# Kernel tuning notes

Measured on AMD Instinct MI355X. Metric: run time of the kernel, lower is better.

The kernel has to match this reference:

```python
import jax, jax.numpy as jnp
import numpy as np

N = 50000
E = 800000
IN_F = 256
ATT_D = 256
H = 8
D_K = ATT_D // H  # 32
NORM_IDX = 0  # opt['attention_norm_idx']


def setup_inputs() -> dict:
    key = jax.random.key(0)
    ks = jax.random.split(key, 10)
    x = jax.random.normal(ks[0], (N, IN_F), dtype=jnp.float32)
    edge = jax.random.randint(ks[1], (2, E), 0, N, dtype=jnp.int64)
    edge_weights = jax.random.uniform(ks[2], (E,), dtype=jnp.float32)
    s = 0.02
    Wq = jax.random.normal(ks[3], (ATT_D, IN_F), dtype=jnp.float32) * s
    bq = jax.random.normal(ks[4], (ATT_D,), dtype=jnp.float32) * s
    Wk = jax.random.normal(ks[5], (ATT_D, IN_F), dtype=jnp.float32) * s
    bk = jax.random.normal(ks[6], (ATT_D,), dtype=jnp.float32) * s
    Wv = jax.random.normal(ks[7], (ATT_D, IN_F), dtype=jnp.float32) * s
    bv = jax.random.normal(ks[8], (ATT_D,), dtype=jnp.float32) * s
    return {"x": x, "edge": edge, "edge_weights": edge_weights,
            "Wq": Wq, "bq": bq, "Wk": Wk, "bk": bk, "Wv": Wv, "bv": bv}


def _segment_softmax(logits, seg, num_segments):
    # scatter-softmax grouped by seg (torch_geometric.utils.softmax semantics)
    m = jax.ops.segment_max(logits, seg, num_segments=num_segments)  # [N, H]
    ex = jnp.exp(logits - m[seg])
    s = jax.ops.segment_sum(ex, seg, num_segments=num_segments)
    return ex / (s[seg] + 1e-16)


def reference(x, edge, edge_weights, Wq, bq, Wk, bk, Wv, bv):
    # Linear projections, then [N, H, D_K] -> transpose to [N, D_K, H]
    q = (x @ Wq.T + bq).reshape(N, H, D_K).transpose(0, 2, 1)
    k = (x @ Wk.T + bk).reshape(N, H, D_K).transpose(0, 2, 1)
    v = (x @ Wv.T + bv).reshape(N, H, D_K).transpose(0, 2, 1)
    src = q[edge[0]]      # [E, D_K, H]
    dst_k = k[edge[1]]    # [E, D_K, H]
    prods = jnp.sum(src * dst_k, axis=1) / np.sqrt(D_K)  # [E, H]
    prods = prods * edge_weights[:, None]
    attention = _segment_softmax(prods, edge[NORM_IDX], N)  # [E, H]
    return attention, v
```

## Files before the change

### kernel.cpp

```cpp
#include <hip/hip_runtime.h>

#define NN 50000
#define EE 800000
#define FF 256
#define HH 8
#define DK 32

typedef short bf16x8 __attribute__((ext_vector_type(8)));
typedef float f32x4  __attribute__((ext_vector_type(4)));

__device__ __forceinline__ float b2f(short s) {
    return __uint_as_float(((unsigned)(unsigned short)s) << 16);
}
__device__ __forceinline__ short f2b(float f) {
    unsigned u = __float_as_uint(f);
    return (short)((u + 0x7fff + ((u >> 16) & 1)) >> 16);
}

__device__ __forceinline__ void gld16(void* lds, const void* g) {
    __builtin_amdgcn_global_load_lds(
        (const __attribute__((address_space(1))) unsigned int*)g,
        (__attribute__((address_space(3))) unsigned int*)lds,
        16, 0, 0);
}

__global__ __launch_bounds__(256) void sniff_all(
    const void* x, const void* ew, const void* wq, const void* bq,
    const void* wk, const void* bk, const void* wv, const void* bv,
    const void* edge, int* __restrict__ flags)
{
    __shared__ int tot;
    if (threadIdx.x == 0) tot = 0;
    __syncthreads();
    int b = blockIdx.x;
    if (b < 8) {
        const void* ptrs[8] = {x, ew, wq, bq, wk, bk, wv, bv};
        const int   ns[8]   = {NN * FF, EE, FF * FF, FF, FF * FF, FF, FF * FF, FF};
        const unsigned short* p = (const unsigned short*)ptrs[b];
        int half = ns[b] >> 1;
        int S = half < 4096 ? half : 4096;
        int cnt = 0;
        for (int i = threadIdx.x; i < S; i += 256) {
            unsigned v = p[2 * i];
            cnt += (((v >> 7) & 0xFF) >= 0xC0) ? 1 : 0;
        }
        atomicAdd(&tot, cnt);
        __syncthreads();
        if (threadIdx.x == 0) flags[b] = (tot * 32 > S) ? 1 : 0;
    } else {
        const unsigned* e32 = (const unsigned*)edge;
        int cnt = 0;
        for (int i = threadIdx.x; i < 4096; i += 256)
            cnt += (e32[2 * i + 1] != 0u) ? 1 : 0;
        atomicAdd(&tot, cnt);
        __syncthreads();
        if (threadIdx.x == 0) flags[8] = (tot < 100) ? 1 : 0;
    }
}

__global__ __launch_bounds__(256) void convert_wb(
    const void* wq, const void* wk, const void* wv,
    const void* bq, const void* bk, const void* bv,
    short* __restrict__ wb, float* __restrict__ bb,
    const int* __restrict__ flags)
{
    int b = blockIdx.x;
    if (b < 96) {
        int mat = b >> 5;
        const void* src = mat == 0 ? wq : mat == 1 ? wk : wv;
        int isf = flags[2 + mat * 2];
        int base = (b & 31) * 2048 + threadIdx.x * 8;
        bf16x8 v;
        if (isf) {
            const f32x4* pp = (const f32x4*)((const float*)src + base);
            f32x4 a = pp[0], c = pp[1];
            #pragma unroll
            for (int j = 0; j < 4; ++j) { v[j] = f2b(a[j]); v[4 + j] = f2b(c[j]); }
        } else {
            v = *(const bf16x8*)((const short*)src + base);
        }
        int row = base >> 8, k = base & 255;
        int s = k >> 5, quad = (k >> 3) & 3;
        int pc = (row << 2) + (quad ^ ((row >> 1) & 3));
        *(bf16x8*)(wb + mat * (FF * FF) + s * 8192 + pc * 8) = v;
    } else {
        #pragma unroll
        for (int mat = 0; mat < 3; ++mat) {
            const void* src = mat == 0 ? bq : mat == 1 ? bk : bv;
            int isf = flags[3 + mat * 2];
            int i = threadIdx.x;
            bb[mat * FF + i] = isf ? ((const float*)src)[i]
                                   : b2f(((const short*)src)[i]);
        }
    }
}

__global__ __launch_bounds__(256) void qkv_gemm(
    const void* __restrict__ x, const short* __restrict__ wb,
    const float* __restrict__ bb, short* __restrict__ qo,
    short* __restrict__ ko, float* __restrict__ vo,
    const int* __restrict__ flags, int mlo, int mhi)
{
    __shared__ __align__(16) short wlds[2][8192];
    const int isf32x = flags[0];
    const int tid = threadIdx.x, wave = tid >> 6, lane = tid & 63;
    const int l16 = lane & 15, quad = lane >> 4;
    const int rows0 = blockIdx.x * 64 + wave * 16;
    const int rowa = rows0 + l16;
    const int rowc = rowa < NN ? rowa : NN - 1;
    const int koff = quad * 8;
    const size_t xrow = (size_t)rowc * FF;

    const int rdo = l16 * 32 + ((quad ^ ((l16 >> 1) & 3)) << 3);

    bf16x8 afrag[8];
    if (isf32x) {
        f32x4 t0[8], t1[8];
        #pragma unroll
        for (int s = 0; s < 8; ++s) {
            const f32x4* p = (const f32x4*)((const float*)x + xrow + s * 32 + koff);
            t0[s] = p[0]; t1[s] = p[1];
        }
        #pragma unroll
        for (int s = 0; s < 8; ++s)
            #pragma unroll
            for (int j = 0; j < 4; ++j) {
                afrag[s][j]     = f2b(t0[s][j]);
                afrag[s][4 + j] = f2b(t1[s][j]);
            }
    } else {
        #pragma unroll
        for (int s = 0; s < 8; ++s)
            afrag[s] = *(const bf16x8*)((const short*)x + xrow + s * 32 + koff);
    }

    #define STAGE(buf, W_, s) do {                                              \
        const short* gs_ = (W_) + (s) * 8192;                                   \
        _Pragma("unroll")                                                       \
        for (int i_ = 0; i_ < 4; ++i_)                                          \
            gld16(&wlds[buf][(i_ * 256 + (tid & ~63)) * 8],                     \
                  gs_ + (size_t)(i_ * 256 + tid) * 8);                          \
    } while (0)

    for (int mat = mlo; mat <= mhi; ++mat) {
        const short* W = wb + mat * (FF * FF);
        if (mat != mlo) __syncthreads();
        STAGE(0, W, 0);
        __syncthreads();

        f32x4 acc[16] = {};
        #pragma unroll
        for (int s = 0; s < 8; ++s) {
            const int cur = s & 1;
            if (s < 7) STAGE(cur ^ 1, W, s + 1);
            const short* ws0 = &wlds[cur][rdo];
            #pragma unroll
            for (int c = 0; c < 16; ++c) {
                bf16x8 bf = *(const bf16x8*)(ws0 + c * 512);
                acc[c] = __builtin_amdgcn_mfma_f32_16x16x32_bf16(afrag[s], bf, acc[c], 0, 0, 0);
            }
            __syncthreads();
        }

        const float* bias = bb + mat * FF;
        short* slice = (short*)wlds + wave * 4096;

        if (mat == 2) {
            float* lsf = (float*)slice;
            #pragma unroll
            for (int h = 0; h < 2; ++h) {
                #pragma unroll
                for (int ci = 0; ci < 8; ++ci) {
                    int c = ci * 2 + h;
                    int col = c * 16 + l16;
                    float bv = bias[col];
                    int pcl = l16 * 8 + ci;
                    #pragma unroll
                    for (int rr = 0; rr < 4; ++rr)
                        lsf[(quad * 4 + rr) * 128 + pcl] = acc[c][rr] + bv;
                }
                #pragma unroll
                for (int it = 0; it < 8; ++it) {
                    int idx = it * 64 + lane;
                    int r = idx >> 5, cc = idx & 31;
                    int row = rows0 + r;
                    if (row < NN)
                        *(f32x4*)(vo + (size_t)row * FF + h * 128 + cc * 4) =
                            ((const f32x4*)lsf)[idx];
                }
            }
        } else {
            #pragma unroll
            for (int c = 0; c < 16; ++c) {
                int col = c * 16 + l16;
                float bv = bias[col];
                #pragma unroll
                for (int rr = 0; rr < 4; ++rr)
                    slice[(quad * 4 + rr) * 256 + col] = f2b(acc[c][rr] + bv);
            }
            short* out = (mat == 0) ? qo : ko;
            #pragma unroll
            for (int it = 0; it < 8; ++it) {
                int idx = it * 64 + lane;
                int r = idx >> 5, cc = idx & 31;
                int row = rows0 + r;
                if (row < NN)
                    *(bf16x8*)(out + (size_t)row * FF + cc * 8) =
                        *(const bf16x8*)(slice + r * 256 + cc * 8);
            }
        }
    }
    #undef STAGE
}

__device__ __forceinline__ float edge_exp_f(
    const int* __restrict__ edge, const void* __restrict__ ew,
    const short* __restrict__ q, const short* __restrict__ k,
    int t, int isf32, int is64, int* s_out)
{
    int e = t >> 3, h = t & 7;
    int s = is64 ? edge[2 * (size_t)e] : edge[e];
    int d = is64 ? edge[2 * ((size_t)EE + e)] : edge[EE + e];
    *s_out = s;
    const short* qp = q + (size_t)s * FF + h * DK;
    const short* kp = k + (size_t)d * FF + h * DK;
    float dot = 0.f;
    #pragma unroll
    for (int i = 0; i < 4; ++i) {
        bf16x8 qa = *(const bf16x8*)(qp + i * 8);
        bf16x8 ka = *(const bf16x8*)(kp + i * 8);
        #pragma unroll
        for (int j = 0; j < 8; ++j) dot += b2f(qa[j]) * b2f(ka[j]);
    }
    float w = isf32 ? ((const float*)ew)[e] : b2f(((const short*)ew)[e]);
    return __expf(dot * 0.17677669529663687f * w);
}

__global__ __launch_bounds__(256) void edge_pass_a(
    const int* __restrict__ edge, const void* __restrict__ ew,
    const short* __restrict__ q, const short* __restrict__ k,
    float* __restrict__ sums, float* __restrict__ expbuf,
    const int* __restrict__ flags, int use_exp)
{
    int t = blockIdx.x * 256 + threadIdx.x;
    int s;
    float exv = edge_exp_f(edge, ew, q, k, t, flags[1], flags[8], &s);
    if (use_exp) expbuf[t] = exv;
    atomicAdd(&sums[s * HH + (threadIdx.x & 7)], exv);
}

__global__ __launch_bounds__(256) void rsum_inv(float* __restrict__ sums)
{
    int i = blockIdx.x * 256 + threadIdx.x;
    if (i < NN * HH) sums[i] = 1.0f / (sums[i] + 1e-16f);
}

__global__ __launch_bounds__(256) void edge_pass_b(
    const int* __restrict__ edge, const void* __restrict__ ew,
    const short* __restrict__ q, const short* __restrict__ k,
    const float* __restrict__ sums, const float* __restrict__ expbuf,
    float* __restrict__ att, const int* __restrict__ flags, int use_exp)
{
    int t = blockIdx.x * 256 + threadIdx.x;
    float exv; int s;
    if (use_exp) {
        int e = t >> 3;
        s = flags[8] ? edge[2 * (size_t)e] : edge[e];
        exv = expbuf[t];
    } else {
        exv = edge_exp_f(edge, ew, q, k, t, flags[1], flags[8], &s);
    }
    att[t] = exv * sums[s * HH + (t & 7)];
}

extern "C" void kernel_launch(void* const* d_in, const int* in_sizes, int n_in,
                              void* d_out, int out_size, void* d_ws, size_t ws_size,
                              hipStream_t stream) {
    const void* x    = d_in[0];
    const int*  edge = (const int*)d_in[1];
    const void* ew   = d_in[2];
    const void* Wq   = d_in[3];
    const void* bq   = d_in[4];
    const void* Wk   = d_in[5];
    const void* bk   = d_in[6];
    const void* Wv   = d_in[7];
    const void* bv   = d_in[8];

    float* att_out = (float*)d_out;
    float* v_out   = att_out + (size_t)EE * HH;

    char*  ws    = (char*)d_ws;
    int*   flags = (int*)ws;
    float* sums  = (float*)(ws + 256);
    const size_t SUMS_B = (size_t)NN * HH * 4;
    const size_t Q_B    = (size_t)NN * FF * 2;
    const size_t EXP_B  = (size_t)EE * HH * 4;
    short* q_  = (short*)(ws + 256 + SUMS_B);
    short* wb  = (short*)(ws + 256 + SUMS_B + Q_B);
    float* bb  = (float*)(ws + 256 + SUMS_B + Q_B + 3 * FF * FF * 2);
    float* expb = (float*)(ws + 256 + SUMS_B + Q_B + 3 * FF * FF * 2 + 3 * FF * 4);
    const size_t BASE_B = 256 + SUMS_B + Q_B + 3 * FF * FF * 2 + 3 * FF * 4;
    const int use_exp = (ws_size >= BASE_B + EXP_B) ? 1 : 0;
    const int fused   = (ws_size >= BASE_B + EXP_B + Q_B) ? 1 : 0;

    sniff_all<<<9, 256, 0, stream>>>(x, ew, Wq, bq, Wk, bk, Wv, bv, edge, flags);
    convert_wb<<<97, 256, 0, stream>>>(Wq, Wk, Wv, bq, bk, bv, wb, bb, flags);
    hipMemsetAsync(sums, 0, SUMS_B, stream);

    const int nEH = EE * HH;
    dim3 g((NN + 63) / 64);

    if (fused) {
        short* k_ = (short*)(ws + BASE_B + EXP_B);
        qkv_gemm<<<g, 256, 0, stream>>>(x, wb, bb, q_, k_, v_out, flags, 0, 2);
        edge_pass_a<<<nEH / 256, 256, 0, stream>>>(edge, ew, q_, k_, sums, expb, flags, 1);
        rsum_inv<<<(NN * HH + 255) / 256, 256, 0, stream>>>(sums);
        edge_pass_b<<<nEH / 256, 256, 0, stream>>>(edge, ew, q_, k_, sums, expb, att_out, flags, 1);
    } else {
        short* k_ = (short*)v_out;
        qkv_gemm<<<g, 256, 0, stream>>>(x, wb, bb, q_, k_, nullptr, flags, 0, 1);
        edge_pass_a<<<nEH / 256, 256, 0, stream>>>(edge, ew, q_, k_, sums, expb, flags, use_exp);
        rsum_inv<<<(NN * HH + 255) / 256, 256, 0, stream>>>(sums);
        edge_pass_b<<<nEH / 256, 256, 0, stream>>>(edge, ew, q_, k_, sums, expb, att_out, flags, use_exp);
        qkv_gemm<<<g, 256, 0, stream>>>(x, wb, bb, nullptr, nullptr, v_out, flags, 2, 2);
    }
}
```

Measured before the change: 336.7 us.

## Split QKV GEMM across blocks per matrix with XCD-aware block swizzle

The QKV projection kernel now assigns each workgroup a single 64-row tile of one weight matrix instead of looping over all three, launching 3x as many 128-thread blocks. Each wave handles 32 rows (two 16-row MFMA fragments sharing each B-fragment LDS read), and block IDs are remapped so neighbouring tiles land on the same XCD for L2 reuse of x. The aim is more parallelism and better weight-fragment reuse per LDS load. The cost is that x rows are reloaded and converted once per matrix rather than once per tile, and there is higher register pressure from doubled accumulators.

```diff
diff --git a/kernel.cpp b/kernel.cpp
--- a/kernel.cpp
+++ b/kernel.cpp
@@ -22,6 +22,12 @@
         (const __attribute__((address_space(1))) unsigned int*)g,
         (__attribute__((address_space(3))) unsigned int*)lds,
         16, 0, 0);
+}
+
+__device__ __forceinline__ int xcd_swz(int bid, int nwg) {
+    int q = nwg >> 3, r = nwg & 7, x = bid & 7, i = bid >> 3;
+    int base = x < r ? x * (q + 1) : r * (q + 1) + (x - r) * q;
+    return base + i;
 }
 
 __global__ __launch_bounds__(256) void sniff_all(
@@ -95,80 +101,88 @@
     }
 }
 
-__global__ __launch_bounds__(256) void qkv_gemm(
+__global__ __launch_bounds__(128, 2) void qkv_gemm(
     const void* __restrict__ x, const short* __restrict__ wb,
     const float* __restrict__ bb, short* __restrict__ qo,
     short* __restrict__ ko, float* __restrict__ vo,
-    const int* __restrict__ flags, int mlo, int mhi)
+    const int* __restrict__ flags, int matbase, int nmats)
 {
     __shared__ __align__(16) short wlds[2][8192];
     const int isf32x = flags[0];
     const int tid = threadIdx.x, wave = tid >> 6, lane = tid & 63;
     const int l16 = lane & 15, quad = lane >> 4;
-    const int rows0 = blockIdx.x * 64 + wave * 16;
-    const int rowa = rows0 + l16;
-    const int rowc = rowa < NN ? rowa : NN - 1;
+
+    const int nwg = 782 * nmats;
+    const int w = xcd_swz(blockIdx.x, nwg);
+    const int xb = w / nmats;
+    const int mat = matbase + (w - xb * nmats);
+
+    const short* W = wb + mat * (FF * FF);
+    const int rows0 = xb * 64 + wave * 32;
+
+    const int rdo = l16 * 32 + ((quad ^ ((l16 >> 1) & 3)) << 3);
     const int koff = quad * 8;
-    const size_t xrow = (size_t)rowc * FF;
-
-    const int rdo = l16 * 32 + ((quad ^ ((l16 >> 1) & 3)) << 3);
-
-    bf16x8 afrag[8];
-    if (isf32x) {
-        f32x4 t0[8], t1[8];
-        #pragma unroll
-        for (int s = 0; s < 8; ++s) {
-            const f32x4* p = (const f32x4*)((const float*)x + xrow + s * 32 + koff);
-            t0[s] = p[0]; t1[s] = p[1];
-        }
-        #pragma unroll
-        for (int s = 0; s < 8; ++s)
-            #pragma unroll
-            for (int j = 0; j < 4; ++j) {
-                afrag[s][j]     = f2b(t0[s][j]);
-                afrag[s][4 + j] = f2b(t1[s][j]);
+
+    bf16x8 afrag[2][8];
+    #pragma unroll
+    for (int rg = 0; rg < 2; ++rg) {
+        const int rowa = rows0 + rg * 16 + l16;
+        const int rowc = rowa < NN ? rowa : NN - 1;
+        const size_t xrow = (size_t)rowc * FF;
+        if (isf32x) {
+            #pragma unroll
+            for (int s = 0; s < 8; ++s) {
+                const f32x4* p = (const f32x4*)((const float*)x + xrow + s * 32 + koff);
+                f32x4 u = p[0], v2 = p[1];
+                #pragma unroll
+                for (int j = 0; j < 4; ++j) {
+                    afrag[rg][s][j]     = f2b(u[j]);
+                    afrag[rg][s][4 + j] = f2b(v2[j]);
+                }
             }
-    } else {
-        #pragma unroll
-        for (int s = 0; s < 8; ++s)
-            afrag[s] = *(const bf16x8*)((const short*)x + xrow + s * 32 + koff);
-    }
-
-    #define STAGE(buf, W_, s) do {                                              \
-        const short* gs_ = (W_) + (s) * 8192;                                   \
+        } else {
+            #pragma unroll
+            for (int s = 0; s < 8; ++s)
+                afrag[rg][s] = *(const bf16x8*)((const short*)x + xrow + s * 32 + koff);
+        }
+    }
+
+    #define STAGE(buf, s) do {                                                  \
+        const short* gs_ = W + (s) * 8192;                                      \
         _Pragma("unroll")                                                       \
-        for (int i_ = 0; i_ < 4; ++i_)                                          \
-            gld16(&wlds[buf][(i_ * 256 + (tid & ~63)) * 8],                     \
-                  gs_ + (size_t)(i_ * 256 + tid) * 8);                          \
+        for (int i_ = 0; i_ < 8; ++i_)                                          \
+            gld16(&wlds[buf][(i_ * 128 + (tid & ~63)) * 8],                     \
+                  gs_ + (size_t)(i_ * 128 + tid) * 8);                          \
     } while (0)
 
-    for (int mat = mlo; mat <= mhi; ++mat) {
-        const short* W = wb + mat * (FF * FF);
-        if (mat != mlo) __syncthreads();
-        STAGE(0, W, 0);
+    STAGE(0, 0);
+    __syncthreads();
+
+    f32x4 acc[2][16] = {};
+    #pragma unroll
+    for (int s = 0; s < 8; ++s) {
+        const int cur = s & 1;
+        if (s < 7) STAGE(cur ^ 1, s + 1);
+        const short* ws0 = &wlds[cur][rdo];
+        #pragma unroll
+        for (int c = 0; c < 16; ++c) {
+            bf16x8 bf = *(const bf16x8*)(ws0 + c * 512);
+            acc[0][c] = __builtin_amdgcn_mfma_f32_16x16x32_bf16(afrag[0][s], bf, acc[0][c], 0, 0, 0);
+            acc[1][c] = __builtin_amdgcn_mfma_f32_16x16x32_bf16(afrag[1][s], bf, acc[1][c], 0, 0, 0);
+        }
         __syncthreads();
-
-        f32x4 acc[16] = {};
-        #pragma unroll
-        for (int s = 0; s < 8; ++s) {
-            const int cur = s & 1;
-            if (s < 7) STAGE(cur ^ 1, W, s + 1);
-            const short* ws0 = &wlds[cur][rdo];
-            #pragma unroll
-            for (int c = 0; c < 16; ++c) {
-                bf16x8 bf = *(const bf16x8*)(ws0 + c * 512);
-                acc[c] = __builtin_amdgcn_mfma_f32_16x16x32_bf16(afrag[s], bf, acc[c], 0, 0, 0);
-            }
-            __syncthreads();
-        }
-
-        const float* bias = bb + mat * FF;
-        short* slice = (short*)wlds + wave * 4096;
-
-        if (mat == 2) {
-            float* lsf = (float*)slice;
-            #pragma unroll
-            for (int h = 0; h < 2; ++h) {
+    }
+    #undef STAGE
+
+    const float* bias = bb + mat * FF;
+    short* slice = (short*)wlds + wave * 8192;
+
+    if (mat == 2) {
+        float* lsf = (float*)slice;
+        #pragma unroll
+        for (int h = 0; h < 2; ++h) {
+            #pragma unroll
+            for (int rg = 0; rg < 2; ++rg)
                 #pragma unroll
                 for (int ci = 0; ci < 8; ++ci) {
                     int c = ci * 2 + h;
@@ -177,40 +191,40 @@
                     int pcl = l16 * 8 + ci;
                     #pragma unroll
                     for (int rr = 0; rr < 4; ++rr)
-                        lsf[(quad * 4 + rr) * 128 + pcl] = acc[c][rr] + bv;
+                        lsf[(rg * 16 + quad * 4 + rr) * 128 + pcl] = acc[rg][c][rr] + bv;
                 }
-                #pragma unroll
-                for (int it = 0; it < 8; ++it) {
-                    int idx = it * 64 + lane;
-                    int r = idx >> 5, cc = idx & 31;
-                    int row = rows0 + r;
-                    if (row < NN)
-                        *(f32x4*)(vo + (size_t)row * FF + h * 128 + cc * 4) =
-                            ((const f32x4*)lsf)[idx];
-                }
+            #pragma unroll
+            for (int it = 0; it < 16; ++it) {
+                int idx = it * 64 + lane;
+                int r = idx >> 5, cc = idx & 31;
+                int row = rows0 + r;
+                if (row < NN)
+                    *(f32x4*)(vo + (size_t)row * FF + h * 128 + cc * 4) =
+                        ((const f32x4*)lsf)[idx];
             }
-        } else {
+        }
+    } else {
+        #pragma unroll
+        for (int rg = 0; rg < 2; ++rg)
             #pragma unroll
             for (int c = 0; c < 16; ++c) {
                 int col = c * 16 + l16;
                 float bv = bias[col];
                 #pragma unroll
                 for (int rr = 0; rr < 4; ++rr)
-                    slice[(quad * 4 + rr) * 256 + col] = f2b(acc[c][rr] + bv);
+                    slice[(rg * 16 + quad * 4 + rr) * 256 + col] = f2b(acc[rg][c][rr] + bv);
             }
-            short* out = (mat == 0) ? qo : ko;
-            #pragma unroll
-            for (int it = 0; it < 8; ++it) {
-                int idx = it * 64 + lane;
-                int r = idx >> 5, cc = idx & 31;
-                int row = rows0 + r;
-                if (row < NN)
-                    *(bf16x8*)(out + (size_t)row * FF + cc * 8) =
-                        *(const bf16x8*)(slice + r * 256 + cc * 8);
-            }
-        }
-    }
-    #undef STAGE
+        short* out = (mat == 0) ? qo : ko;
+        #pragma unroll
+        for (int it = 0; it < 16; ++it) {
+            int idx = it * 64 + lane;
+            int r = idx >> 5, cc = idx & 31;
+            int row = rows0 + r;
+            if (row < NN)
+                *(bf16x8*)(out + (size_t)row * FF + cc * 8) =
+                    *(const bf16x8*)(slice + r * 256 + cc * 8);
+        }
+    }
 }
 
 __device__ __forceinline__ float edge_exp_f(
@@ -308,20 +322,19 @@
     hipMemsetAsync(sums, 0, SUMS_B, stream);
 
     const int nEH = EE * HH;
-    dim3 g((NN + 63) / 64);
 
     if (fused) {
         short* k_ = (short*)(ws + BASE_B + EXP_B);
-        qkv_gemm<<<g, 256, 0, stream>>>(x, wb, bb, q_, k_, v_out, flags, 0, 2);
+        qkv_gemm<<<782 * 3, 128, 0, stream>>>(x, wb, bb, q_, k_, v_out, flags, 0, 3);
         edge_pass_a<<<nEH / 256, 256, 0, stream>>>(edge, ew, q_, k_, sums, expb, flags, 1);
         rsum_inv<<<(NN * HH + 255) / 256, 256, 0, stream>>>(sums);
         edge_pass_b<<<nEH / 256, 256, 0, stream>>>(edge, ew, q_, k_, sums, expb, att_out, flags, 1);
     } else {
         short* k_ = (short*)v_out;
-        qkv_gemm<<<g, 256, 0, stream>>>(x, wb, bb, q_, k_, nullptr, flags, 0, 1);
+        qkv_gemm<<<782 * 2, 128, 0, stream>>>(x, wb, bb, q_, k_, nullptr, flags, 0, 2);
         edge_pass_a<<<nEH / 256, 256, 0, stream>>>(edge, ew, q_, k_, sums, expb, flags, use_exp);
         rsum_inv<<<(NN * HH + 255) / 256, 256, 0, stream>>>(sums);
         edge_pass_b<<<nEH / 256, 256, 0, stream>>>(edge, ew, q_, k_, sums, expb, att_out, flags, use_exp);
-        qkv_gemm<<<g, 256, 0, stream>>>(x, wb, bb, nullptr, nullptr, v_out, flags, 2, 2);
-    }
-}
+        qkv_gemm<<<782, 128, 0, stream>>>(x, wb, bb, nullptr, nullptr, v_out, flags, 2, 1);
+    }
+}
```

Measured after the change: 304.2 us. 1.11x faster.
